# Optimization experiments

Hardware: AMD Instinct MI355X
Metric: run time of the kernel (lower is better)

## Reference

```python
import jax, jax.numpy as jnp
import numpy as np

EMBED = 1024
HEAD = 128
B, T = 4, 4096


def setup_inputs() -> dict:
    key = jax.random.key(0)
    k1, k2, k3, k4 = jax.random.split(key, 4)
    context = jax.random.normal(k1, (B, T, EMBED), dtype=jnp.float32)
    # nn.Linear(embedding_size, head_size, bias=False): y = x @ W^T; store W^T as [C, H]
    s = 1.0 / np.sqrt(EMBED)
    Wk = jax.random.normal(k2, (EMBED, HEAD), dtype=jnp.float32) * s
    Wq = jax.random.normal(k3, (EMBED, HEAD), dtype=jnp.float32) * s
    Wv = jax.random.normal(k4, (EMBED, HEAD), dtype=jnp.float32) * s
    return {"context": context, "Wk": Wk, "Wq": Wq, "Wv": Wv}


def reference(context, Wk, Wq, Wv):
    Bc, Tc, C = context.shape
    k = jnp.einsum("btc,ch->bth", context, Wk)
    q = jnp.einsum("btc,ch->bth", context, Wq)
    v = jnp.einsum("btc,ch->bth", context, Wv)
    # NOTE: original scales by 1/sqrt(C) (embedding size), not 1/sqrt(head_size)
    scale = 1.0 / jnp.sqrt(jnp.float32(C))
    scores = jnp.einsum("bqh,bkh->bqk", q, k) * scale  # [B, T, T]
    causal = jnp.tril(jnp.ones((Tc, Tc), dtype=bool))
    scores = jnp.where(causal, scores, -jnp.inf)
    attn = jax.nn.softmax(scores, axis=-1)
    # dropout_rate = 0.0 (eval-mode): no-op
    out = jnp.einsum("bqk,bkh->bqh", attn, v)
    return out
```

## Files before the change

kernel.cpp:

```cpp
#include <hip/hip_runtime.h>
#include <cstdint>
#include <cstddef>

#define EMBED 1024
#define HEAD  128
#define BATCH 4
#define SEQ   4096
#define KSC   0.04508422f

typedef __attribute__((ext_vector_type(4))) float f32x4;
typedef __attribute__((ext_vector_type(16))) float f32x16;
typedef __attribute__((ext_vector_type(8))) short s16x8;
typedef __attribute__((ext_vector_type(4))) int i32x4;
typedef __attribute__((ext_vector_type(4))) unsigned short u16x4;

__device__ __forceinline__ unsigned short f2bf(float f) {
    union { float f; unsigned u; } v; v.f = f;
    unsigned r = v.u + 0x7fffu + ((v.u >> 16) & 1u);
    return (unsigned short)(r >> 16);
}

__device__ __forceinline__ int cvtpk(float lo, float hi_) {
    int r;
    asm("v_cvt_pk_bf16_f32 %0, %1, %2" : "=v"(r) : "v"(lo), "v"(hi_));
    return r;
}

__global__ __launch_bounds__(256) void wt_kernel(const float* __restrict__ Wq,
                                                 const float* __restrict__ Wk,
                                                 const float* __restrict__ Wv,
                                                 unsigned short* __restrict__ Wt) {
    int idx = blockIdx.x * 256 + threadIdx.x;
    int sel = idx >> 17;
    int r   = idx & 131071;
    const float* W = (sel == 0) ? Wq : (sel == 1) ? Wk : Wv;
    int h = r >> 10, k = r & 1023;
    Wt[(size_t)(sel * 128 + h) * EMBED + k] = f2bf(W[(size_t)k * HEAD + h]);
}

__global__ __launch_bounds__(512) void proj_kernel(const float* __restrict__ ctx,
                                                   const unsigned short* __restrict__ Wt,
                                                   unsigned short* __restrict__ QKV) {
    __shared__ __align__(16) short As[64 * 72];
    __shared__ __align__(16) short Bs[384 * 72];
    const int tid = threadIdx.x;
    const int lane = tid & 63, w = tid >> 6;
    const int wr = w >> 2, wc = w & 3;
    const int lr = lane & 15, lk = lane >> 4;
    const int m0 = blockIdx.x * 64;

    f32x4 zero = {0.f, 0.f, 0.f, 0.f};
    f32x4 acc[2][6];
    #pragma unroll
    for (int i = 0; i < 2; ++i)
        #pragma unroll
        for (int jn = 0; jn < 6; ++jn) acc[i][jn] = zero;

    for (int kk = 0; kk < EMBED; kk += 64) {
        __syncthreads();
        {
            int row = tid >> 3, cg = tid & 7;
            const float* src = ctx + (size_t)(m0 + row) * EMBED + kk + cg * 8;
            f32x4 x0 = *(const f32x4*)src;
            f32x4 x1 = *(const f32x4*)(src + 4);
            s16x8 cv;
            cv[0] = (short)f2bf(x0[0]); cv[1] = (short)f2bf(x0[1]);
            cv[2] = (short)f2bf(x0[2]); cv[3] = (short)f2bf(x0[3]);
            cv[4] = (short)f2bf(x1[0]); cv[5] = (short)f2bf(x1[1]);
            cv[6] = (short)f2bf(x1[2]); cv[7] = (short)f2bf(x1[3]);
            *(s16x8*)&As[row * 72 + cg * 8] = cv;
        }
        #pragma unroll
        for (int jb = 0; jb < 6; ++jb) {
            int c = tid + jb * 512;
            int row = c >> 3, cg = c & 7;
            *(s16x8*)&Bs[row * 72 + cg * 8] =
                *(const s16x8*)(Wt + (size_t)row * EMBED + kk + cg * 8);
        }
        __syncthreads();
        s16x8 af[2][2], bfr[6][2];
        #pragma unroll
        for (int mi = 0; mi < 2; ++mi)
            #pragma unroll
            for (int k2 = 0; k2 < 2; ++k2)
                af[mi][k2] = *(const s16x8*)&As[(wr * 32 + mi * 16 + lr) * 72 + k2 * 32 + lk * 8];
        #pragma unroll
        for (int ni = 0; ni < 6; ++ni)
            #pragma unroll
            for (int k2 = 0; k2 < 2; ++k2)
                bfr[ni][k2] = *(const s16x8*)&Bs[(wc * 96 + ni * 16 + lr) * 72 + k2 * 32 + lk * 8];
        #pragma unroll
        for (int k2 = 0; k2 < 2; ++k2)
            #pragma unroll
            for (int mi = 0; mi < 2; ++mi)
                #pragma unroll
                for (int ni = 0; ni < 6; ++ni)
                    acc[mi][ni] = __builtin_amdgcn_mfma_f32_16x16x32_bf16(af[mi][k2], bfr[ni][k2], acc[mi][ni], 0, 0, 0);
    }
    #pragma unroll
    for (int mi = 0; mi < 2; ++mi) {
        int row = m0 + wr * 32 + mi * 16 + lk * 4;
        #pragma unroll
        for (int ni = 0; ni < 6; ++ni) {
            int n0 = wc * 96 + ni * 16;
            unsigned short* dst = QKV + (size_t)(n0 >> 7) * 2097152 + (n0 & 127) + lr;
            #pragma unroll
            for (int r = 0; r < 4; ++r)
                dst[(size_t)(row + r) * HEAD] = f2bf(acc[mi][ni][r]);
        }
    }
}

__global__ __launch_bounds__(256) void vt_kernel(const unsigned short* __restrict__ V,
                                                 unsigned short* __restrict__ Vt) {
    __shared__ __align__(16) unsigned short L[64][136];
    const int tid = threadIdx.x;
    const int t0 = blockIdx.x * 64;
    const int b  = t0 >> 12;
    const int tl = t0 & (SEQ - 1);
    #pragma unroll
    for (int j = 0; j < 4; ++j) {
        int c = tid + j * 256;
        int row = c >> 4, cg = c & 15;
        *(s16x8*)&L[row][cg * 8] =
            *(const s16x8*)(V + (size_t)(t0 + row) * HEAD + cg * 8);
    }
    __syncthreads();
    #pragma unroll
    for (int j = 0; j < 4; ++j) {
        int c = tid + j * 256;
        int h = c >> 3, tg = c & 7;
        s16x8 y;
        #pragma unroll
        for (int e = 0; e < 8; ++e) y[e] = (short)L[tg * 8 + e][h];
        *(s16x8*)(Vt + ((size_t)b * HEAD + h) * SEQ + tl + tg * 8) = y;
    }
}

__global__ __launch_bounds__(256, 2) void attn_kernel(const unsigned short* __restrict__ Q,
                                                      const unsigned short* __restrict__ K,
                                                      const unsigned short* __restrict__ Vt,
                                                      unsigned short* __restrict__ po,
                                                      float* __restrict__ pml) {
    __shared__ __align__(16) char smem[65536];
    const int tid = threadIdx.x;
    const int lane = tid & 63, w = tid >> 6;
    const int l31 = lane & 31, hi = lane >> 5;
    const int hi16 = hi << 4;

    const int b = blockIdx.x / 272;
    int t = blockIdx.x % 272;
    int qt = 0, cum = 0;
    while (cum + ((qt >> 1) + 1) <= t) { cum += (qt >> 1) + 1; ++qt; }
    const int c = t - cum;
    const int nj = min(4, 2 * qt + 2 - 4 * c);
    const int kb0 = c * 256;
    const int slot = b * 272 + cum + c;

    const unsigned short* qp = Q + ((size_t)(b * SEQ + qt * 128 + w * 32 + l31)) * HEAD + hi * 8;
    s16x8 qf[8];
    #pragma unroll
    for (int dt = 0; dt < 8; ++dt) qf[dt] = *(const s16x8*)(qp + dt * 16);

    f32x16 o0, o1, o2, o3;
    #pragma unroll
    for (int r = 0; r < 16; ++r) { o0[r] = 0.f; o1[r] = 0.f; o2[r] = 0.f; o3[r] = 0.f; }
    float m_run = -1e30f, l_run = 0.f;

    const int krow = tid >> 4, kch = tid & 15;
    const int vdr  = tid >> 3, vch = tid & 7;

    s16x8 kst[4], vst[4];
    #pragma unroll
    for (int p = 0; p < 4; ++p) {
        kst[p] = *(const s16x8*)(K + ((size_t)(b * SEQ + kb0 + krow + p * 16)) * HEAD + kch * 8);
        vst[p] = *(const s16x8*)(Vt + ((size_t)(b * HEAD + vdr + p * 32)) * SEQ + kb0 + vch * 8);
    }
    #pragma unroll
    for (int p = 0; p < 4; ++p) {
        int r0 = krow + p * 16;
        *(s16x8*)(smem + r0 * 256 + ((kch * 16) ^ ((r0 & 7) << 4))) = kst[p];
        int d0 = vdr + p * 32;
        *(s16x8*)(smem + 16384 + d0 * 128 + ((vch * 16) ^ ((d0 & 7) << 4))) = vst[p];
    }
    __syncthreads();

    for (int j = 0; j < nj; ++j) {
        const int cur = j & 1;
        const int cb = cur * 32768;
        const int kb = kb0 + j * 64;
        if (j + 1 < nj) {
            int kbn = kb + 64;
            #pragma unroll
            for (int p = 0; p < 4; ++p) {
                kst[p] = *(const s16x8*)(K + ((size_t)(b * SEQ + kbn + krow + p * 16)) * HEAD + kch * 8);
                vst[p] = *(const s16x8*)(Vt + ((size_t)(b * HEAD + vdr + p * 32)) * SEQ + kbn + vch * 8);
            }
        }

        f32x16 st0, st1;
        #pragma unroll
        for (int r = 0; r < 16; ++r) { st0[r] = 0.f; st1[r] = 0.f; }
        const int sw = (l31 & 7) << 4;
        const char* kbase0 = smem + cb + l31 * 256;
        const char* kbase1 = kbase0 + 32 * 256;
        __builtin_amdgcn_s_setprio(1);
        #pragma unroll
        for (int dt = 0; dt < 8; ++dt) {
            s16x8 ka0 = *(const s16x8*)(kbase0 + ((dt * 32 + hi16) ^ sw));
            s16x8 ka1 = *(const s16x8*)(kbase1 + ((dt * 32 + hi16) ^ sw));
            st0 = __builtin_amdgcn_mfma_f32_32x32x16_bf16(ka0, qf[dt], st0, 0, 0, 0);
            st1 = __builtin_amdgcn_mfma_f32_32x32x16_bf16(ka1, qf[dt], st1, 0, 0, 0);
        }
        __builtin_amdgcn_s_setprio(0);

        if (4 * c + j >= 2 * qt) {
            const int qg = qt * 128 + w * 32 + l31;
            #pragma unroll
            for (int r = 0; r < 16; ++r) {
                int crow = (r & 3) + 8 * (r >> 2) + 4 * hi;
                if (kb + crow > qg)      st0[r] = -3e37f;
                if (kb + 32 + crow > qg) st1[r] = -3e37f;
            }
        }

        float mx = st0[0];
        #pragma unroll
        for (int r = 1; r < 16; ++r) mx = fmaxf(mx, st0[r]);
        #pragma unroll
        for (int r = 0; r < 16; ++r) mx = fmaxf(mx, st1[r]);
        mx = fmaxf(mx, __shfl_xor(mx, 32));
        float mt = mx * KSC;
        if (!__all(mt <= m_run + 8.0f)) {
            float mn = fmaxf(m_run, mt);
            float f = exp2f(m_run - mn);
            l_run *= f;
            int fi = __float_as_int(f);
            #pragma unroll
            for (int r = 0; r < 16; ++r) {
                int srcb = 4 * ((r & 3) + 8 * (r >> 2)) + 16 * hi;
                float fr = __int_as_float(__builtin_amdgcn_ds_bpermute(srcb, fi));
                o0[r] *= fr; o1[r] *= fr; o2[r] *= fr; o3[r] *= fr;
            }
            m_run = mn;
        }
        float rs = 0.f;
        #pragma unroll
        for (int r = 0; r < 16; ++r) {
            st0[r] = exp2f(fmaf(st0[r], KSC, -m_run)); rs += st0[r];
            st1[r] = exp2f(fmaf(st1[r], KSC, -m_run)); rs += st1[r];
        }
        rs += __shfl_xor(rs, 32);
        l_run += rs;

        int a0 = cvtpk(st0[0], st0[1]),   b0 = cvtpk(st0[4], st0[5]);
        int a1 = cvtpk(st0[2], st0[3]),   b1 = cvtpk(st0[6], st0[7]);
        int a2 = cvtpk(st0[8], st0[9]),   b2 = cvtpk(st0[12], st0[13]);
        int a3 = cvtpk(st0[10], st0[11]), b3 = cvtpk(st0[14], st0[15]);
        int a4 = cvtpk(st1[0], st1[1]),   b4 = cvtpk(st1[4], st1[5]);
        int a5 = cvtpk(st1[2], st1[3]),   b5 = cvtpk(st1[6], st1[7]);
        int a6 = cvtpk(st1[8], st1[9]),   b6 = cvtpk(st1[12], st1[13]);
        int a7 = cvtpk(st1[10], st1[11]), b7 = cvtpk(st1[14], st1[15]);
        asm volatile("v_permlane32_swap_b32 %0, %1" : "+v"(a0), "+v"(b0));
        asm volatile("v_permlane32_swap_b32 %0, %1" : "+v"(a1), "+v"(b1));
        asm volatile("v_permlane32_swap_b32 %0, %1" : "+v"(a2), "+v"(b2));
        asm volatile("v_permlane32_swap_b32 %0, %1" : "+v"(a3), "+v"(b3));
        asm volatile("v_permlane32_swap_b32 %0, %1" : "+v"(a4), "+v"(b4));
        asm volatile("v_permlane32_swap_b32 %0, %1" : "+v"(a5), "+v"(b5));
        asm volatile("v_permlane32_swap_b32 %0, %1" : "+v"(a6), "+v"(b6));
        asm volatile("v_permlane32_swap_b32 %0, %1" : "+v"(a7), "+v"(b7));
        i32x4 pw0 = {a0, a1, b0, b1}; s16x8 pa0 = *(s16x8*)&pw0;
        i32x4 pw1 = {a2, a3, b2, b3}; s16x8 pa1 = *(s16x8*)&pw1;
        i32x4 pw2 = {a4, a5, b4, b5}; s16x8 pa2 = *(s16x8*)&pw2;
        i32x4 pw3 = {a6, a7, b6, b7}; s16x8 pa3 = *(s16x8*)&pw3;

        __builtin_amdgcn_s_setprio(1);
        #define PV_NT(oo, nt) { \
            const int vr = (nt) * 32 + l31; \
            const int vsw = (vr & 7) << 4; \
            const char* vb = smem + cb + 16384 + vr * 128; \
            oo = __builtin_amdgcn_mfma_f32_32x32x16_bf16(pa0, *(const s16x8*)(vb + ((0  + hi16) ^ vsw)), oo, 0, 0, 0); \
            oo = __builtin_amdgcn_mfma_f32_32x32x16_bf16(pa1, *(const s16x8*)(vb + ((32 + hi16) ^ vsw)), oo, 0, 0, 0); \
            oo = __builtin_amdgcn_mfma_f32_32x32x16_bf16(pa2, *(const s16x8*)(vb + ((64 + hi16) ^ vsw)), oo, 0, 0, 0); \
            oo = __builtin_amdgcn_mfma_f32_32x32x16_bf16(pa3, *(const s16x8*)(vb + ((96 + hi16) ^ vsw)), oo, 0, 0, 0); }
        PV_NT(o0, 0) PV_NT(o1, 1) PV_NT(o2, 2) PV_NT(o3, 3)
        #undef PV_NT
        __builtin_amdgcn_s_setprio(0);

        if (j + 1 < nj) {
            const int nb = (cur ^ 1) * 32768;
            #pragma unroll
            for (int p = 0; p < 4; ++p) {
                int r0 = krow + p * 16;
                *(s16x8*)(smem + nb + r0 * 256 + ((kch * 16) ^ ((r0 & 7) << 4))) = kst[p];
                int d0 = vdr + p * 32;
                *(s16x8*)(smem + nb + 16384 + d0 * 128 + ((vch * 16) ^ ((d0 & 7) << 4))) = vst[p];
            }
        }
        __syncthreads();
    }

    unsigned short* pob = po + (size_t)slot * 16384;
    #define STORE_NT(oo, nt) { \
        _Pragma("unroll") \
        for (int r = 0; r < 16; ++r) { \
            int qin = w * 32 + (r & 3) + 8 * (r >> 2) + 4 * hi; \
            pob[qin * 128 + (nt) * 32 + l31] = f2bf(oo[r]); \
        } }
    STORE_NT(o0, 0) STORE_NT(o1, 1) STORE_NT(o2, 2) STORE_NT(o3, 3)
    #undef STORE_NT
    if (lane < 32) {
        float* pm = pml + (size_t)slot * 256 + (w * 32 + lane) * 2;
        pm[0] = m_run; pm[1] = l_run;
    }
}

__global__ __launch_bounds__(256) void combine_kernel(const unsigned short* __restrict__ po,
                                                      const float* __restrict__ pml,
                                                      float* __restrict__ out) {
    const int tid = threadIdx.x;
    const int row = blockIdx.x * 8 + (tid >> 5);
    const int l32 = tid & 31;
    const int b = row >> 12, q = row & 4095;
    const int qt = q >> 7, qr = q & 127;
    const int nc = (q >> 8) + 1;
    const int cum = ((qt >> 1) + (qt & 1)) * ((qt >> 1) + 1);
    const size_t bslot = (size_t)b * 272 + cum;

    float M = -1e30f;
    for (int cc = 0; cc < nc; ++cc)
        M = fmaxf(M, pml[(bslot + cc) * 256 + qr * 2]);
    float L = 0.f;
    f32x4 acc = {0.f, 0.f, 0.f, 0.f};
    for (int cc = 0; cc < nc; ++cc) {
        const float* pm = pml + (bslot + cc) * 256 + qr * 2;
        float wgt = exp2f(pm[0] - M);
        L += wgt * pm[1];
        u16x4 x = *(const u16x4*)(po + (bslot + cc) * 16384 + qr * 128 + l32 * 4);
        #pragma unroll
        for (int e = 0; e < 4; ++e) {
            union { unsigned u; float f; } cv; cv.u = ((unsigned)x[e]) << 16;
            acc[e] += wgt * cv.f;
        }
    }
    float inv = 1.f / L;
    f32x4 y = {acc[0] * inv, acc[1] * inv, acc[2] * inv, acc[3] * inv};
    *(f32x4*)(out + (size_t)row * HEAD + l32 * 4) = y;
}

extern "C" void kernel_launch(void* const* d_in, const int* in_sizes, int n_in,
                              void* d_out, int out_size, void* d_ws, size_t ws_size,
                              hipStream_t stream) {
    const float* ctx = (const float*)d_in[0];
    const float* Wk  = (const float*)d_in[1];
    const float* Wq  = (const float*)d_in[2];
    const float* Wv  = (const float*)d_in[3];
    float* out = (float*)d_out;

    unsigned short* Wt  = (unsigned short*)d_ws;
    unsigned short* Qb  = Wt + 3 * 131072;
    unsigned short* Kb  = Qb + 2097152;
    unsigned short* Vb  = Kb + 2097152;
    unsigned short* Vtb = Vb + 2097152;
    unsigned short* po  = Vtb + 2097152;
    float* pml = (float*)(po + (size_t)1088 * 16384);

    wt_kernel<<<1536, 256, 0, stream>>>(Wq, Wk, Wv, Wt);
    proj_kernel<<<256, 512, 0, stream>>>(ctx, Wt, Qb);
    vt_kernel<<<256, 256, 0, stream>>>(Vb, Vtb);
    attn_kernel<<<1088, 256, 0, stream>>>(Qb, Kb, Vtb, po, pml);
    combine_kernel<<<2048, 256, 0, stream>>>(po, pml, out);
}
```

Before: 175.4 us.

## Retile projection GEMM per output matrix and single-buffer attention LDS for occupancy

The projection kernel changes from 64-row by 384-column tiles with 512 threads to 128x128 tiles with 256 threads, using a 2D grid over the Q/K/V outputs. This reuses each context tile across a full 128-column output instead of loading a big 384-row weight slab per block. The attention kernel drops its double-buffered 64KB LDS to a single 32KB buffer and raises launch bounds to 4 blocks per CU. It adds an extra barrier before overwriting the shared tile, so the LDS-write overlap is traded for higher occupancy. The projection also now converts the context tile three times, once per output matrix.

```diff
diff --git a/kernel.cpp b/kernel.cpp
--- a/kernel.cpp
+++ b/kernel.cpp
@@ -38,28 +38,32 @@
     Wt[(size_t)(sel * 128 + h) * EMBED + k] = f2bf(W[(size_t)k * HEAD + h]);
 }
 
-__global__ __launch_bounds__(512) void proj_kernel(const float* __restrict__ ctx,
+__global__ __launch_bounds__(256) void proj_kernel(const float* __restrict__ ctx,
                                                    const unsigned short* __restrict__ Wt,
                                                    unsigned short* __restrict__ QKV) {
-    __shared__ __align__(16) short As[64 * 72];
-    __shared__ __align__(16) short Bs[384 * 72];
+    __shared__ __align__(16) short As[128 * 72];
+    __shared__ __align__(16) short Bs[128 * 72];
     const int tid = threadIdx.x;
     const int lane = tid & 63, w = tid >> 6;
-    const int wr = w >> 2, wc = w & 3;
+    const int wr = w >> 1, wc = w & 1;
     const int lr = lane & 15, lk = lane >> 4;
-    const int m0 = blockIdx.x * 64;
+    const int m0 = blockIdx.x * 128;
+    const unsigned short* Wts = Wt + (size_t)blockIdx.y * 131072;
+    unsigned short* outp = QKV + (size_t)blockIdx.y * 2097152;
 
     f32x4 zero = {0.f, 0.f, 0.f, 0.f};
-    f32x4 acc[2][6];
-    #pragma unroll
-    for (int i = 0; i < 2; ++i)
-        #pragma unroll
-        for (int jn = 0; jn < 6; ++jn) acc[i][jn] = zero;
+    f32x4 acc[4][4];
+    #pragma unroll
+    for (int i = 0; i < 4; ++i)
+        #pragma unroll
+        for (int jn = 0; jn < 4; ++jn) acc[i][jn] = zero;
 
     for (int kk = 0; kk < EMBED; kk += 64) {
         __syncthreads();
-        {
-            int row = tid >> 3, cg = tid & 7;
+        #pragma unroll
+        for (int t = 0; t < 4; ++t) {
+            int c = tid + t * 256;
+            int row = c >> 3, cg = c & 7;
             const float* src = ctx + (size_t)(m0 + row) * EMBED + kk + cg * 8;
             f32x4 x0 = *(const f32x4*)src;
             f32x4 x1 = *(const f32x4*)(src + 4);
@@ -69,44 +73,38 @@
             cv[4] = (short)f2bf(x1[0]); cv[5] = (short)f2bf(x1[1]);
             cv[6] = (short)f2bf(x1[2]); cv[7] = (short)f2bf(x1[3]);
             *(s16x8*)&As[row * 72 + cg * 8] = cv;
-        }
-        #pragma unroll
-        for (int jb = 0; jb < 6; ++jb) {
-            int c = tid + jb * 512;
-            int row = c >> 3, cg = c & 7;
             *(s16x8*)&Bs[row * 72 + cg * 8] =
-                *(const s16x8*)(Wt + (size_t)row * EMBED + kk + cg * 8);
+                *(const s16x8*)(Wts + (size_t)row * EMBED + kk + cg * 8);
         }
         __syncthreads();
-        s16x8 af[2][2], bfr[6][2];
-        #pragma unroll
-        for (int mi = 0; mi < 2; ++mi)
+        s16x8 af[4][2], bfr[4][2];
+        #pragma unroll
+        for (int mi = 0; mi < 4; ++mi)
             #pragma unroll
             for (int k2 = 0; k2 < 2; ++k2)
-                af[mi][k2] = *(const s16x8*)&As[(wr * 32 + mi * 16 + lr) * 72 + k2 * 32 + lk * 8];
-        #pragma unroll
-        for (int ni = 0; ni < 6; ++ni)
+                af[mi][k2] = *(const s16x8*)&As[(wr * 64 + mi * 16 + lr) * 72 + k2 * 32 + lk * 8];
+        #pragma unroll
+        for (int ni = 0; ni < 4; ++ni)
             #pragma unroll
             for (int k2 = 0; k2 < 2; ++k2)
-                bfr[ni][k2] = *(const s16x8*)&Bs[(wc * 96 + ni * 16 + lr) * 72 + k2 * 32 + lk * 8];
+                bfr[ni][k2] = *(const s16x8*)&Bs[(wc * 64 + ni * 16 + lr) * 72 + k2 * 32 + lk * 8];
         #pragma unroll
         for (int k2 = 0; k2 < 2; ++k2)
             #pragma unroll
-            for (int mi = 0; mi < 2; ++mi)
+            for (int mi = 0; mi < 4; ++mi)
                 #pragma unroll
-                for (int ni = 0; ni < 6; ++ni)
+                for (int ni = 0; ni < 4; ++ni)
                     acc[mi][ni] = __builtin_amdgcn_mfma_f32_16x16x32_bf16(af[mi][k2], bfr[ni][k2], acc[mi][ni], 0, 0, 0);
     }
     #pragma unroll
-    for (int mi = 0; mi < 2; ++mi) {
-        int row = m0 + wr * 32 + mi * 16 + lk * 4;
-        #pragma unroll
-        for (int ni = 0; ni < 6; ++ni) {
-            int n0 = wc * 96 + ni * 16;
-            unsigned short* dst = QKV + (size_t)(n0 >> 7) * 2097152 + (n0 & 127) + lr;
+    for (int mi = 0; mi < 4; ++mi) {
+        int row = m0 + wr * 64 + mi * 16 + lk * 4;
+        #pragma unroll
+        for (int ni = 0; ni < 4; ++ni) {
+            int col = wc * 64 + ni * 16 + lr;
             #pragma unroll
             for (int r = 0; r < 4; ++r)
-                dst[(size_t)(row + r) * HEAD] = f2bf(acc[mi][ni][r]);
+                outp[(size_t)(row + r) * HEAD + col] = f2bf(acc[mi][ni][r]);
         }
     }
 }
@@ -137,12 +135,12 @@
     }
 }
 
-__global__ __launch_bounds__(256, 2) void attn_kernel(const unsigned short* __restrict__ Q,
+__global__ __launch_bounds__(256, 4) void attn_kernel(const unsigned short* __restrict__ Q,
                                                       const unsigned short* __restrict__ K,
                                                       const unsigned short* __restrict__ Vt,
                                                       unsigned short* __restrict__ po,
                                                       float* __restrict__ pml) {
-    __shared__ __align__(16) char smem[65536];
+    __shared__ __align__(16) char smem[32768];
     const int tid = threadIdx.x;
     const int lane = tid & 63, w = tid >> 6;
     const int l31 = lane & 31, hi = lane >> 5;
@@ -186,8 +184,6 @@
     __syncthreads();
 
     for (int j = 0; j < nj; ++j) {
-        const int cur = j & 1;
-        const int cb = cur * 32768;
         const int kb = kb0 + j * 64;
         if (j + 1 < nj) {
             int kbn = kb + 64;
@@ -202,7 +198,7 @@
         #pragma unroll
         for (int r = 0; r < 16; ++r) { st0[r] = 0.f; st1[r] = 0.f; }
         const int sw = (l31 & 7) << 4;
-        const char* kbase0 = smem + cb + l31 * 256;
+        const char* kbase0 = smem + l31 * 256;
         const char* kbase1 = kbase0 + 32 * 256;
         __builtin_amdgcn_s_setprio(1);
         #pragma unroll
@@ -278,7 +274,7 @@
         #define PV_NT(oo, nt) { \
             const int vr = (nt) * 32 + l31; \
             const int vsw = (vr & 7) << 4; \
-            const char* vb = smem + cb + 16384 + vr * 128; \
+            const char* vb = smem + 16384 + vr * 128; \
             oo = __builtin_amdgcn_mfma_f32_32x32x16_bf16(pa0, *(const s16x8*)(vb + ((0  + hi16) ^ vsw)), oo, 0, 0, 0); \
             oo = __builtin_amdgcn_mfma_f32_32x32x16_bf16(pa1, *(const s16x8*)(vb + ((32 + hi16) ^ vsw)), oo, 0, 0, 0); \
             oo = __builtin_amdgcn_mfma_f32_32x32x16_bf16(pa2, *(const s16x8*)(vb + ((64 + hi16) ^ vsw)), oo, 0, 0, 0); \
@@ -288,16 +284,16 @@
         __builtin_amdgcn_s_setprio(0);
 
         if (j + 1 < nj) {
-            const int nb = (cur ^ 1) * 32768;
+            __syncthreads();
             #pragma unroll
             for (int p = 0; p < 4; ++p) {
                 int r0 = krow + p * 16;
-                *(s16x8*)(smem + nb + r0 * 256 + ((kch * 16) ^ ((r0 & 7) << 4))) = kst[p];
+                *(s16x8*)(smem + r0 * 256 + ((kch * 16) ^ ((r0 & 7) << 4))) = kst[p];
                 int d0 = vdr + p * 32;
-                *(s16x8*)(smem + nb + 16384 + d0 * 128 + ((vch * 16) ^ ((d0 & 7) << 4))) = vst[p];
+                *(s16x8*)(smem + 16384 + d0 * 128 + ((vch * 16) ^ ((d0 & 7) << 4))) = vst[p];
             }
-        }
-        __syncthreads();
+            __syncthreads();
+        }
     }
 
     unsigned short* pob = po + (size_t)slot * 16384;
@@ -366,7 +362,7 @@
     float* pml = (float*)(po + (size_t)1088 * 16384);
 
     wt_kernel<<<1536, 256, 0, stream>>>(Wq, Wk, Wv, Wt);
-    proj_kernel<<<256, 512, 0, stream>>>(ctx, Wt, Qb);
+    proj_kernel<<<dim3(128, 3), 256, 0, stream>>>(ctx, Wt, Qb);
     vt_kernel<<<256, 256, 0, stream>>>(Vb, Vtb);
     attn_kernel<<<1088, 256, 0, stream>>>(Qb, Kb, Vtb, po, pml);
     combine_kernel<<<2048, 256, 0, stream>>>(po, pml, out);
```

Measured after the change: 258.2 us. 47.2% more time.
